# Performance work log

Measured on AMD Instinct MI355X. Metric: run time of the kernel, lower is better.

The kernel has to match this reference:

```python
import jax, jax.numpy as jnp
import numpy as np

# Module hyperparameters (see init_kwargs)
P1, P2 = 32, 32      # num_patches_h, num_patches_w (256/8)
H1, W2 = 8, 8        # patch_size
CH = 3               # input channels
CI, SI = 768, 4      # num_cores, rfs_per_capsule (capsule_size=256, rf_size=64)
KOUT, LOUT = 256, 4  # output_cores, slots per output core
PROBA = 0.1          # connection_proba


def setup_inputs() -> dict:
    key = jax.random.key(0)
    kx, kc = jax.random.split(key)
    x = jax.random.normal(kx, (128, 256, 256, 3), dtype=jnp.float32)
    # fast_scrramble: fixed random-sparse binary connectivity tensor
    # [source_core, source_slot, dest_core, dest_slot]
    C = jax.random.bernoulli(kc, PROBA, (CI, SI, KOUT, LOUT)).astype(jnp.float32)
    return {"x": x, "C": C}


def reference(x, C):
    b = x.shape[0]
    # 'b (p1 h1) (p2 w2) c -> b p1 p2 h1 w2 c'
    x = x.reshape(b, P1, H1, P2, W2, CH).transpose(0, 1, 3, 2, 4, 5)
    # 'b p1 p2 h1 w2 c -> b h1 w2 (p1 p2 c)'
    x = x.transpose(0, 3, 4, 1, 2, 5).reshape(b, H1, W2, P1 * P2 * CH)
    # 'b h1 w2 (ci si) -> b ci si h1 w2'
    x = x.reshape(b, H1, W2, CI, SI).transpose(0, 3, 4, 1, 2)
    # Literal einsum from the source: no shared labels between operands,
    # so this is sum_{c,s} x (per b,h,w) times sum_{i,j} C (per k,l).
    return jnp.einsum('bcshw,ijkl->bklhw', x, C)
```

## Files before the change

### kernel.cpp

```cpp
#include <hip/hip_runtime.h>


#define ROWSUM_ELEMS (128 * 8 * 768)
#define PSC_ELEMS    (96 * 1024)

__global__ __launch_bounds__(256) void reduce_C_part(const float* __restrict__ C,
                                                     float4* __restrict__ psC) {
    const int p = blockIdx.x;
    const int t = threadIdx.x;
    const float4* row = (const float4*)C + (size_t)p * 32 * 256 + t;
    float4 a = {0.f, 0.f, 0.f, 0.f};
#pragma unroll
    for (int r = 0; r < 32; ++r) {
        float4 v = row[(size_t)r * 256];
        a.x += v.x; a.y += v.y; a.z += v.z; a.w += v.w;
    }
    psC[p * 256 + t] = a;
}

__global__ __launch_bounds__(192) void reduce_rows(const float* __restrict__ x,
                                                   float4* __restrict__ rowsum) {
    const int blk = blockIdx.x;
    const int b = blk >> 3, h = blk & 7;
    const int t = threadIdx.x;
    const float4* xb = (const float4*)x + (size_t)b * 49152 + (size_t)h * 192 + t;
    float4 a = {0.f, 0.f, 0.f, 0.f};
#pragma unroll
    for (int j = 0; j < 32; ++j) {
        float4 v = xb[(size_t)j * 1536];
        a.x += v.x; a.y += v.y; a.z += v.z; a.w += v.w;
    }
    rowsum[(size_t)blk * 192 + t] = a;
}

__global__ __launch_bounds__(128) void finalize(const float* __restrict__ rowsum,
                                                const float* __restrict__ psC,
                                                float* __restrict__ sx,
                                                float* __restrict__ sC) {
    const int blk = blockIdx.x, t = threadIdx.x;
    if (blk < 128) {
        if (t < 64) {
            const int h = t >> 3, w = t & 7;
            const float* r = rowsum + (size_t)blk * 6144 + h * 768 + 3 * w;
            float s = 0.f;
#pragma unroll
            for (int g = 0; g < 32; ++g)
                s += r[24 * g] + r[24 * g + 1] + r[24 * g + 2];
            sx[blk * 64 + t] = s;
        }
    } else {
        const int col = (blk - 128) * 128 + t;
        float s = 0.f;
#pragma unroll
        for (int p = 0; p < 96; ++p) s += psC[p * 1024 + col];
        sC[col] = s;
    }
}

__global__ __launch_bounds__(256) void expand_kernel(const float* __restrict__ sx,
                                                     const float* __restrict__ sC,
                                                     float4* __restrict__ out) {
    const int b = blockIdx.y, bx = blockIdx.x, t = threadIdx.x;
    __shared__ float sxl[64];
    __shared__ float sCl[64];
    if (t < 64)       sxl[t]      = sx[b * 64 + t];
    else if (t < 128) sCl[t - 64] = sC[bx * 64 + (t - 64)];
    __syncthreads();

    const float4 v = ((const float4*)sxl)[t & 15];
    float4* ob = out + (size_t)b * 16384 + bx * 1024 + t;
#pragma unroll
    for (int u = 0; u < 4; ++u) {
        const float s = sCl[(t >> 4) + 16 * u];
        float4 rr; rr.x = v.x * s; rr.y = v.y * s; rr.z = v.z * s; rr.w = v.w * s;
        ob[256 * u] = rr;
    }
}

extern "C" void kernel_launch(void* const* d_in, const int* in_sizes, int n_in,
                              void* d_out, int out_size, void* d_ws, size_t ws_size,
                              hipStream_t stream) {
    const float* x = (const float*)d_in[0];
    const float* C = (const float*)d_in[1];
    float* out = (float*)d_out;

    float* rowsum = (float*)d_ws;
    float* psC    = rowsum + ROWSUM_ELEMS;
    float* sC     = psC + PSC_ELEMS;
    float* sx     = sC + 1024;

    reduce_C_part<<<dim3(96),      256, 0, stream>>>(C, (float4*)psC);
    reduce_rows  <<<dim3(1024),    192, 0, stream>>>(x, (float4*)rowsum);
    finalize     <<<dim3(136),     128, 0, stream>>>(rowsum, psC, sx, sC);
    expand_kernel<<<dim3(16, 128), 256, 0, stream>>>(sx, sC, (float4*)out);
}
```

Measured before the change: 192.4 us.

## Fuse row reduction, finalize and expand into one cooperative grid-synced kernel

```diff
diff --git a/kernel.cpp b/kernel.cpp
--- a/kernel.cpp
+++ b/kernel.cpp
@@ -1,7 +1,10 @@
 #include <hip/hip_runtime.h>
+#include <hip/hip_cooperative_groups.h>
+
+namespace cg = cooperative_groups;
 
 
-#define ROWSUM_ELEMS (128 * 8 * 768)
+#define ROWSUM_ELEMS (512 * 8 * 768)
 #define PSC_ELEMS    (96 * 1024)
 
 __global__ __launch_bounds__(256) void reduce_C_part(const float* __restrict__ C,
@@ -18,62 +21,77 @@
     psC[p * 256 + t] = a;
 }
 
-__global__ __launch_bounds__(192) void reduce_rows(const float* __restrict__ x,
-                                                   float4* __restrict__ rowsum) {
-    const int blk = blockIdx.x;
-    const int b = blk >> 3, h = blk & 7;
-    const int t = threadIdx.x;
-    const float4* xb = (const float4*)x + (size_t)b * 49152 + (size_t)h * 192 + t;
-    float4 a = {0.f, 0.f, 0.f, 0.f};
-#pragma unroll
-    for (int j = 0; j < 32; ++j) {
-        float4 v = xb[(size_t)j * 1536];
-        a.x += v.x; a.y += v.y; a.z += v.z; a.w += v.w;
-    }
-    rowsum[(size_t)blk * 192 + t] = a;
-}
-
-__global__ __launch_bounds__(128) void finalize(const float* __restrict__ rowsum,
+__global__ __launch_bounds__(384, 3) void fused(const float4* __restrict__ x4,
+                                                float4* __restrict__ rowsum4,
                                                 const float* __restrict__ psC,
                                                 float* __restrict__ sx,
-                                                float* __restrict__ sC) {
-    const int blk = blockIdx.x, t = threadIdx.x;
+                                                float* __restrict__ sC,
+                                                float4* __restrict__ out4) {
+    cg::grid_group grid = cg::this_grid();
+    const int blk = blockIdx.x;
+    const int t   = threadIdx.x;
+    __shared__ float lds[64][5];
+
+    {
+        const int b = blk >> 2, q = blk & 3;
+        const float4* base = x4 + (size_t)b * 49152 + q * 12288 + t;
+        float4 acc[4];
+#pragma unroll
+        for (int j = 0; j < 4; ++j) acc[j] = (float4){0.f, 0.f, 0.f, 0.f};
+#pragma unroll
+        for (int m = 0; m < 32; ++m) {
+            float4 v = base[m * 384];
+            const int j = m & 3;
+            acc[j].x += v.x; acc[j].y += v.y; acc[j].z += v.z; acc[j].w += v.w;
+        }
+        const int r = t / 192, c4 = t % 192;
+        float4* dst = rowsum4 + (size_t)blk * 1536 + r * 192 + c4;
+#pragma unroll
+        for (int j = 0; j < 4; ++j) dst[j * 384] = acc[j];
+    }
+    grid.sync();
+
     if (blk < 128) {
-        if (t < 64) {
-            const int h = t >> 3, w = t & 7;
-            const float* r = rowsum + (size_t)blk * 6144 + h * 768 + 3 * w;
+        if (t < 256) {
+            const int hw = t & 63, part = t >> 6;
+            const int h = hw >> 3, w = hw & 7;
+            const float* rp = (const float*)rowsum4
+                            + (((size_t)blk * 4 + part) * 8 + h) * 768 + 3 * w;
             float s = 0.f;
 #pragma unroll
             for (int g = 0; g < 32; ++g)
-                s += r[24 * g] + r[24 * g + 1] + r[24 * g + 2];
-            sx[blk * 64 + t] = s;
+                s += rp[24 * g] + rp[24 * g + 1] + rp[24 * g + 2];
+            lds[hw][part] = s;
         }
-    } else {
-        const int col = (blk - 128) * 128 + t;
-        float s = 0.f;
+        __syncthreads();
+        if (t < 64) sx[blk * 64 + t] = lds[t][0] + lds[t][1] + lds[t][2] + lds[t][3];
+    } else if (blk < 136) {
+        if (t < 128) {
+            const int col = (blk - 128) * 128 + t;
+            float s = 0.f;
 #pragma unroll
-        for (int p = 0; p < 96; ++p) s += psC[p * 1024 + col];
-        sC[col] = s;
+            for (int p = 0; p < 96; ++p) s += psC[p * 1024 + col];
+            sC[col] = s;
+        }
     }
-}
+    grid.sync();
 
-__global__ __launch_bounds__(256) void expand_kernel(const float* __restrict__ sx,
-                                                     const float* __restrict__ sC,
-                                                     float4* __restrict__ out) {
-    const int b = blockIdx.y, bx = blockIdx.x, t = threadIdx.x;
-    __shared__ float sxl[64];
-    __shared__ float sCl[64];
-    if (t < 64)       sxl[t]      = sx[b * 64 + t];
-    else if (t < 128) sCl[t - 64] = sC[bx * 64 + (t - 64)];
-    __syncthreads();
-
-    const float4 v = ((const float4*)sxl)[t & 15];
-    float4* ob = out + (size_t)b * 16384 + bx * 1024 + t;
+    {
+        const int g0  = blk * 384 + t;
+        const int rem = g0 & 16383;
+        const int b0  = g0 >> 14;
+        const float s = sC[rem >> 4];
+        const float4* sx4 = (const float4*)sx;
 #pragma unroll
-    for (int u = 0; u < 4; ++u) {
-        const float s = sCl[(t >> 4) + 16 * u];
-        float4 rr; rr.x = v.x * s; rr.y = v.y * s; rr.z = v.z * s; rr.w = v.w * s;
-        ob[256 * u] = rr;
+        for (int i = 0; i < 11; ++i) {
+            const int b = b0 + 12 * i;
+            if (b < 128) {
+                const float4 v = sx4[b * 16 + (rem & 15)];
+                float4 rr;
+                rr.x = v.x * s; rr.y = v.y * s; rr.z = v.z * s; rr.w = v.w * s;
+                out4[(size_t)b * 16384 + rem] = rr;
+            }
+        }
     }
 }
 
@@ -82,15 +100,20 @@
                               hipStream_t stream) {
     const float* x = (const float*)d_in[0];
     const float* C = (const float*)d_in[1];
-    float* out = (float*)d_out;
 
     float* rowsum = (float*)d_ws;
     float* psC    = rowsum + ROWSUM_ELEMS;
     float* sC     = psC + PSC_ELEMS;
     float* sx     = sC + 1024;
 
-    reduce_C_part<<<dim3(96),      256, 0, stream>>>(C, (float4*)psC);
-    reduce_rows  <<<dim3(1024),    192, 0, stream>>>(x, (float4*)rowsum);
-    finalize     <<<dim3(136),     128, 0, stream>>>(rowsum, psC, sx, sC);
-    expand_kernel<<<dim3(16, 128), 256, 0, stream>>>(sx, sC, (float4*)out);
+    reduce_C_part<<<dim3(96), 256, 0, stream>>>(C, (float4*)psC);
+
+    const float4* x4 = (const float4*)x;
+    float4* rowsum4  = (float4*)rowsum;
+    float4* out4     = (float4*)d_out;
+    const float* psCc = psC;
+    void* args[] = {(void*)&x4, (void*)&rowsum4, (void*)&psCc,
+                    (void*)&sx, (void*)&sC, (void*)&out4};
+    hipLaunchCooperativeKernel((const void*)fused, dim3(512), dim3(384),
+                               args, 0, stream);
 }
```

Result: slower. 316.6 us (+64.5%).

## Restructure x reduction into per-segment LDS-binned partials with nontemporal loads/stores

Applied to the files above, without the earlier changes.

```diff
diff --git a/kernel.cpp b/kernel.cpp
--- a/kernel.cpp
+++ b/kernel.cpp
@@ -1,51 +1,76 @@
 #include <hip/hip_runtime.h>
 
+typedef float f4 __attribute__((ext_vector_type(4)));
 
-#define ROWSUM_ELEMS (128 * 8 * 768)
-#define PSC_ELEMS    (96 * 1024)
 
-__global__ __launch_bounds__(256) void reduce_C_part(const float* __restrict__ C,
-                                                     float4* __restrict__ psC) {
-    const int p = blockIdx.x;
-    const int t = threadIdx.x;
-    const float4* row = (const float4*)C + (size_t)p * 32 * 256 + t;
-    float4 a = {0.f, 0.f, 0.f, 0.f};
+#define PSX_ELEMS (1536 * 64)
+#define PSC_ELEMS (96 * 1024)
+
+__global__ __launch_bounds__(256) void k1_reduce(const f4* __restrict__ x4,
+                                                 float* __restrict__ psx,
+                                                 f4* __restrict__ psC) {
+    const int bk = blockIdx.x, t = threadIdx.x;
+
+    if (bk < 1536) {
+        const int b = bk / 12, seg = bk % 12;
+        const int off = seg * 256 + t;
+        const f4* xb = x4 + (size_t)b * 49152 + off;
+
+        f4 acc0 = {0.f,0.f,0.f,0.f}, acc1 = {0.f,0.f,0.f,0.f};
+        f4 acc2 = {0.f,0.f,0.f,0.f}, acc3 = {0.f,0.f,0.f,0.f};
 #pragma unroll
-    for (int r = 0; r < 32; ++r) {
-        float4 v = row[(size_t)r * 256];
-        a.x += v.x; a.y += v.y; a.z += v.z; a.w += v.w;
+        for (int k = 0; k < 16; k += 4) {
+            f4 v0 = __builtin_nontemporal_load(xb + (size_t)(k + 0) * 3072);
+            f4 v1 = __builtin_nontemporal_load(xb + (size_t)(k + 1) * 3072);
+            f4 v2 = __builtin_nontemporal_load(xb + (size_t)(k + 2) * 3072);
+            f4 v3 = __builtin_nontemporal_load(xb + (size_t)(k + 3) * 3072);
+            acc0 += v0; acc1 += v1; acc2 += v2; acc3 += v3;
+        }
+        const f4 a = (acc0 + acc1) + (acc2 + acc3);
+
+        __shared__ float bins[64];
+        if (t < 64) bins[t] = 0.f;
+        __syncthreads();
+
+        const int h  = (off / 192) & 7;
+        const int p0 = (4 * off) % 24;
+        atomicAdd(&bins[h * 8 + ((p0 + 0) % 24) / 3], a.x);
+        atomicAdd(&bins[h * 8 + ((p0 + 1) % 24) / 3], a.y);
+        atomicAdd(&bins[h * 8 + ((p0 + 2) % 24) / 3], a.z);
+        atomicAdd(&bins[h * 8 + ((p0 + 3) % 24) / 3], a.w);
+        __syncthreads();
+
+        if (t < 64) psx[(size_t)bk * 64 + t] = bins[t];
+    } else {
+        const int p = bk - 1536;
+        const f4* row = (const f4*)psC;
+        (void)row;
+        const f4* Crow = ((const f4*)nullptr);
+        (void)Crow;
     }
+}
+
+__global__ __launch_bounds__(256) void k1_reduce_C(const f4* __restrict__ C4,
+                                                   f4* __restrict__ psC) {
+    const int p = blockIdx.x, t = threadIdx.x;
+    const f4* row = C4 + (size_t)p * 32 * 256 + t;
+    f4 a = {0.f,0.f,0.f,0.f};
+#pragma unroll
+    for (int r = 0; r < 32; ++r) a += row[(size_t)r * 256];
     psC[p * 256 + t] = a;
 }
 
-__global__ __launch_bounds__(192) void reduce_rows(const float* __restrict__ x,
-                                                   float4* __restrict__ rowsum) {
-    const int blk = blockIdx.x;
-    const int b = blk >> 3, h = blk & 7;
-    const int t = threadIdx.x;
-    const float4* xb = (const float4*)x + (size_t)b * 49152 + (size_t)h * 192 + t;
-    float4 a = {0.f, 0.f, 0.f, 0.f};
-#pragma unroll
-    for (int j = 0; j < 32; ++j) {
-        float4 v = xb[(size_t)j * 1536];
-        a.x += v.x; a.y += v.y; a.z += v.z; a.w += v.w;
-    }
-    rowsum[(size_t)blk * 192 + t] = a;
-}
-
-__global__ __launch_bounds__(128) void finalize(const float* __restrict__ rowsum,
-                                                const float* __restrict__ psC,
-                                                float* __restrict__ sx,
-                                                float* __restrict__ sC) {
+__global__ __launch_bounds__(128) void k2_finalize(const float* __restrict__ psx,
+                                                   const float* __restrict__ psC,
+                                                   float* __restrict__ sx,
+                                                   float* __restrict__ sC) {
     const int blk = blockIdx.x, t = threadIdx.x;
     if (blk < 128) {
         if (t < 64) {
-            const int h = t >> 3, w = t & 7;
-            const float* r = rowsum + (size_t)blk * 6144 + h * 768 + 3 * w;
             float s = 0.f;
 #pragma unroll
-            for (int g = 0; g < 32; ++g)
-                s += r[24 * g] + r[24 * g + 1] + r[24 * g + 2];
+            for (int seg = 0; seg < 12; ++seg)
+                s += psx[((size_t)blk * 12 + seg) * 64 + t];
             sx[blk * 64 + t] = s;
         }
     } else {
@@ -57,9 +82,9 @@
     }
 }
 
-__global__ __launch_bounds__(256) void expand_kernel(const float* __restrict__ sx,
-                                                     const float* __restrict__ sC,
-                                                     float4* __restrict__ out) {
+__global__ __launch_bounds__(256) void k3_expand(const float* __restrict__ sx,
+                                                 const float* __restrict__ sC,
+                                                 f4* __restrict__ out4) {
     const int b = blockIdx.y, bx = blockIdx.x, t = threadIdx.x;
     __shared__ float sxl[64];
     __shared__ float sCl[64];
@@ -67,30 +92,29 @@
     else if (t < 128) sCl[t - 64] = sC[bx * 64 + (t - 64)];
     __syncthreads();
 
-    const float4 v = ((const float4*)sxl)[t & 15];
-    float4* ob = out + (size_t)b * 16384 + bx * 1024 + t;
+    const f4 v = ((const f4*)sxl)[t & 15];
+    f4* ob = out4 + (size_t)b * 16384 + bx * 1024 + t;
 #pragma unroll
     for (int u = 0; u < 4; ++u) {
         const float s = sCl[(t >> 4) + 16 * u];
-        float4 rr; rr.x = v.x * s; rr.y = v.y * s; rr.z = v.z * s; rr.w = v.w * s;
-        ob[256 * u] = rr;
+        f4 rr = v * s;
+        __builtin_nontemporal_store(rr, ob + 256 * u);
     }
 }
 
 extern "C" void kernel_launch(void* const* d_in, const int* in_sizes, int n_in,
                               void* d_out, int out_size, void* d_ws, size_t ws_size,
                               hipStream_t stream) {
-    const float* x = (const float*)d_in[0];
-    const float* C = (const float*)d_in[1];
-    float* out = (float*)d_out;
+    const f4* x4 = (const f4*)d_in[0];
+    const f4* C4 = (const f4*)d_in[1];
 
-    float* rowsum = (float*)d_ws;
-    float* psC    = rowsum + ROWSUM_ELEMS;
-    float* sC     = psC + PSC_ELEMS;
-    float* sx     = sC + 1024;
+    float* psx = (float*)d_ws;
+    float* psC = psx + PSX_ELEMS;
+    float* sC  = psC + PSC_ELEMS;
+    float* sx  = sC + 1024;
 
-    reduce_C_part<<<dim3(96),      256, 0, stream>>>(C, (float4*)psC);
-    reduce_rows  <<<dim3(1024),    192, 0, stream>>>(x, (float4*)rowsum);
-    finalize     <<<dim3(136),     128, 0, stream>>>(rowsum, psC, sx, sC);
-    expand_kernel<<<dim3(16, 128), 256, 0, stream>>>(sx, sC, (float4*)out);
+    k1_reduce  <<<dim3(1536),    256, 0, stream>>>(x4, psx, (f4*)psC);
+    k1_reduce_C<<<dim3(96),      256, 0, stream>>>(C4, (f4*)psC);
+    k2_finalize<<<dim3(136),     128, 0, stream>>>(psx, psC, sx, sC);
+    k3_expand  <<<dim3(16, 128), 256, 0, stream>>>(sx, sC, (f4*)d_out);
 }
```

Result: faster. 182.2 us (-5.3%).
